# Optimization experiments

Measured on AMD Instinct MI355X. Metric: run time of the kernel, lower is better.

Reference implementation:

```python
import jax, jax.numpy as jnp
import numpy as np

N_NODES = 50000
N_FEAT = 128
N_BLOCKS = 4
N_EDGES = 800000  # ~avg degree 16 per hop
OUT_FEAT = 128


def setup_inputs() -> dict:
    key = jax.random.key(0)
    k1, k2, k3, k4, k5, k6 = jax.random.split(key, 6)
    x = jax.random.normal(k1, (N_NODES, N_FEAT), dtype=jnp.float32)
    edge_rows = jax.random.randint(k2, (N_BLOCKS, N_EDGES), 0, N_NODES, dtype=jnp.int64)
    edge_cols = jax.random.randint(k3, (N_BLOCKS, N_EDGES), 0, N_NODES, dtype=jnp.int64)
    edge_vals = jax.random.uniform(k4, (N_BLOCKS, N_EDGES), dtype=jnp.float32)
    shared_weight = jax.random.normal(k5, (N_FEAT * N_BLOCKS, OUT_FEAT), dtype=jnp.float32) * (1.0 / np.sqrt(OUT_FEAT))
    output_bias = jax.random.normal(k6, (OUT_FEAT,), dtype=jnp.float32) * (1.0 / np.sqrt(OUT_FEAT))
    return {"x": x, "edge_rows": edge_rows, "edge_cols": edge_cols,
            "edge_vals": edge_vals, "shared_weight": shared_weight,
            "output_bias": output_bias}


def reference(x, edge_rows, edge_cols, edge_vals, shared_weight, output_bias):
    # Per-hop spmm: AX_i[r] = sum_e vals[e] * x[cols[e]] scattered to rows[e]
    n = x.shape[0]

    def spmm(rows, cols, vals):
        return jax.ops.segment_sum(vals[:, None] * x[cols], rows, num_segments=n)

    hops = jax.vmap(spmm)(edge_rows, edge_cols, edge_vals)  # [B, N, F]
    # torch.cat(feature_output, 1) -> [N, B*F] with hop-major feature blocks
    cat = jnp.transpose(hops, (1, 0, 2)).reshape(n, -1)
    return cat @ shared_weight + output_bias
```

## Files before the change

### kernel.cpp

```cpp
#include <hip/hip_runtime.h>
#include <hip/hip_bf16.h>
#include <type_traits>


#define NBUK_MAX 800
#define RCAP 8192
#define NBLK 512

typedef __attribute__((ext_vector_type(8))) short short8;
typedef __attribute__((ext_vector_type(4))) float f32x4;

static __device__ __forceinline__ ushort f2bf(float f) {
  __hip_bfloat16 h = __float2bfloat16(f);
  return *(ushort*)&h;
}
static __device__ __forceinline__ float bf2f(ushort u) {
  return __uint_as_float(((unsigned)u) << 16);
}

__global__ __launch_bounds__(256) void hist2_kernel(
    const int* __restrict__ rows, int* __restrict__ cnt,
    int* __restrict__ cnt2, unsigned ntot, int nbuk, unsigned chunk)
{
  __shared__ int lcnt[NBUK_MAX];
  for (int i = threadIdx.x; i < nbuk; i += 256) lcnt[i] = 0;
  __syncthreads();
  const unsigned beg = blockIdx.x * chunk;
  const unsigned end = (beg + chunk < ntot) ? (beg + chunk) : ntot;
  if (beg < end) {
    const unsigned q0 = beg >> 2, q1 = end >> 2;
    for (unsigned i = q0 + threadIdx.x; i < q1; i += 256) {
      const int4 r4 = ((const int4*)rows)[i];
      atomicAdd(&lcnt[((unsigned)r4.x) >> 6], 1);
      atomicAdd(&lcnt[((unsigned)r4.y) >> 6], 1);
      atomicAdd(&lcnt[((unsigned)r4.z) >> 6], 1);
      atomicAdd(&lcnt[((unsigned)r4.w) >> 6], 1);
    }
  }
  __syncthreads();
  int* myrow = cnt2 + (size_t)blockIdx.x * nbuk;
  for (int i = threadIdx.x; i < nbuk; i += 256) {
    const int c = lcnt[i];
    myrow[i] = c;
    if (c) atomicAdd(&cnt[i], c);
  }
}

__global__ __launch_bounds__(1024) void scan2_kernel(
    const int* __restrict__ cnt, int* __restrict__ pstartX,
    int* __restrict__ row_start, int nbuk, int n, unsigned ntot)
{
  __shared__ int buf[1024];
  const int t = threadIdx.x;
  const int c = (t < nbuk) ? cnt[t] : 0;
  buf[t] = c;
  __syncthreads();
  for (int off = 1; off < 1024; off <<= 1) {
    const int add = (t >= off) ? buf[t - off] : 0;
    __syncthreads();
    buf[t] += add;
    __syncthreads();
  }
  if (t < nbuk) pstartX[t] = buf[t] - c;
  if (t == 0) row_start[n] = (int)ntot;
}

__global__ __launch_bounds__(256) void scanB_kernel(
    const int* __restrict__ cnt2, const int* __restrict__ pstartX,
    int* __restrict__ bstart2, int nbuk)
{
  const int bk = blockIdx.x * 4 + (threadIdx.x >> 6);
  if (bk >= nbuk) return;
  const int lane = threadIdx.x & 63;
  int v[8];
  int lanesum = 0;
#pragma unroll
  for (int i = 0; i < 8; ++i) {
    v[i] = cnt2[(size_t)(lane * 8 + i) * nbuk + bk];
    lanesum += v[i];
  }
  int incl = lanesum;
#pragma unroll
  for (int off = 1; off < 64; off <<= 1) {
    const int t = __shfl_up(incl, off);
    if (lane >= off) incl += t;
  }
  int run = pstartX[bk] + (incl - lanesum);
#pragma unroll
  for (int i = 0; i < 8; ++i) {
    bstart2[(size_t)(lane * 8 + i) * nbuk + bk] = run;
    run += v[i];
  }
}

__global__ __launch_bounds__(256) void bscatter2_kernel(
    const int* __restrict__ rows, const int* __restrict__ cols,
    const float* __restrict__ vals, const int* __restrict__ bstart2,
    uint2* __restrict__ staged, unsigned ntot, unsigned epb, int nbuk,
    unsigned chunk)
{
  __shared__ int bcnt[NBUK_MAX];
  __shared__ int lcur[NBUK_MAX];
  __shared__ uint2 bins[NBUK_MAX * 8];
  {
    const int* myrow = bstart2 + (size_t)blockIdx.x * nbuk;
    for (int i = threadIdx.x; i < nbuk; i += 256) {
      bcnt[i] = 0;
      lcur[i] = myrow[i];
    }
  }
  __syncthreads();

  const unsigned beg = blockIdx.x * chunk;
  const unsigned end = (beg + chunk < ntot) ? (beg + chunk) : ntot;

  auto push = [&](unsigned r, unsigned c, unsigned hop, float v) {
    const uint2 pay = make_uint2((r << 16) | c, (hop << 30) | __float_as_uint(v));
    const int bk = (int)(r >> 6);
    const int p = atomicAdd(&bcnt[bk], 1);
    if (p < 8) bins[bk * 8 + p] = pay;
    else {
      const int gp = atomicAdd(&lcur[bk], 1);
      staged[gp] = pay;
    }
  };

  for (unsigned base = beg; base < end; base += 2048) {
    const unsigned e0 = base + threadIdx.x * 8u;
    if (e0 + 7 < end) {
#pragma unroll
      for (int g = 0; g < 2; ++g) {
        const unsigned eg = e0 + (unsigned)g * 4u;
        const int4 r4 = *(const int4*)(rows + eg);
        const int4 c4 = *(const int4*)(cols + eg);
        const float4 v4 = *(const float4*)(vals + eg);
#pragma unroll
        for (int q = 0; q < 4; ++q) {
          const unsigned e = eg + q;
          const unsigned hop = (e >= 2u * epb) ? ((e >= 3u * epb) ? 3u : 2u)
                                               : ((e >= epb) ? 1u : 0u);
          push((unsigned)((&r4.x)[q]), (unsigned)((&c4.x)[q]), hop, (&v4.x)[q]);
        }
      }
    } else {
      for (unsigned e = e0; e < end && e < e0 + 8; ++e) {
        const unsigned hop = (e >= 2u * epb) ? ((e >= 3u * epb) ? 3u : 2u)
                                             : ((e >= epb) ? 1u : 0u);
        push((unsigned)rows[e], (unsigned)cols[e], hop, vals[e]);
      }
    }
    __syncthreads();
    for (int bk = threadIdx.x; bk < nbuk; bk += 256) {
      if (bcnt[bk] >= 8) {
        const int gp = lcur[bk];
        uint2* dst = staged + gp;
#pragma unroll
        for (int q = 0; q < 8; ++q) dst[q] = bins[bk * 8 + q];
        lcur[bk] = gp + 8;
        bcnt[bk] = 0;
      }
    }
    __syncthreads();
  }
  for (int bk = threadIdx.x; bk < nbuk; bk += 256) {
    const int c = bcnt[bk];
    if (c > 0) {
      const int gp = lcur[bk];
      for (int q = 0; q < c; ++q) staged[gp + q] = bins[bk * 8 + q];
    }
  }
}

__global__ __launch_bounds__(256) void prep_kernel(
    const float* __restrict__ X, const float* __restrict__ W,
    ushort* __restrict__ Xb, ushort* __restrict__ Wt, int nx8)
{
  const int t = blockIdx.x * 256 + threadIdx.x;
  if (t < nx8) {
    const float4 v0 = ((const float4*)X)[t * 2];
    const float4 v1 = ((const float4*)X)[t * 2 + 1];
    ushort4 o0, o1;
    o0.x = f2bf(v0.x); o0.y = f2bf(v0.y); o0.z = f2bf(v0.z); o0.w = f2bf(v0.w);
    o1.x = f2bf(v1.x); o1.y = f2bf(v1.y); o1.z = f2bf(v1.z); o1.w = f2bf(v1.w);
    ((ushort4*)Xb)[t * 2] = o0;
    ((ushort4*)Xb)[t * 2 + 1] = o1;
  } else if (t < nx8 + 8192) {
    const int u = t - nx8;
    const int gc = u >> 4;
    const int f0 = (u & 15) * 8;
    const float* src = W + (size_t)((gc >> 7) * 128) * 128 + (gc & 127);
    ushort4 o0, o1;
    o0.x = f2bf(src[(size_t)(f0 + 0) * 128]);
    o0.y = f2bf(src[(size_t)(f0 + 1) * 128]);
    o0.z = f2bf(src[(size_t)(f0 + 2) * 128]);
    o0.w = f2bf(src[(size_t)(f0 + 3) * 128]);
    o1.x = f2bf(src[(size_t)(f0 + 4) * 128]);
    o1.y = f2bf(src[(size_t)(f0 + 5) * 128]);
    o1.z = f2bf(src[(size_t)(f0 + 6) * 128]);
    o1.w = f2bf(src[(size_t)(f0 + 7) * 128]);
    ((ushort4*)(Wt + (size_t)gc * 128 + f0))[0] = o0;
    ((ushort4*)(Wt + (size_t)gc * 128 + f0))[1] = o1;
  }
}

__global__ __launch_bounds__(256) void mfma_gemm_kernel(
    const ushort* __restrict__ Xb, const ushort* __restrict__ Wt,
    ushort* __restrict__ Y, int n)
{
  const int w = threadIdx.x >> 6;
  const int l = threadIdx.x & 63;
  const int r16 = l & 15;
  const int kg = l >> 4;
  const int row0 = blockIdx.y * 64 + w * 16;
  const int c0 = blockIdx.x * 64;

  const int gra = min(row0 + r16, n - 1);
  const ushort* ap = Xb + (size_t)gra * 128 + kg * 8;
  const ushort* bp = Wt + (size_t)(c0 + r16) * 128 + kg * 8;

  f32x4 acc[4] = {};
#pragma unroll
  for (int k0 = 0; k0 < 128; k0 += 32) {
    const short8 a = *(const short8*)(ap + k0);
#pragma unroll
    for (int ct = 0; ct < 4; ++ct) {
      const short8 b = *(const short8*)(bp + (size_t)ct * 16 * 128 + k0);
      acc[ct] = __builtin_amdgcn_mfma_f32_16x16x32_bf16(a, b, acc[ct], 0, 0, 0);
    }
  }
  const int rs0 = row0 + kg * 4;
#pragma unroll
  for (int ct = 0; ct < 4; ++ct) {
    const int col = c0 + ct * 16 + r16;
#pragma unroll
    for (int r = 0; r < 4; ++r) {
      const int rs = rs0 + r;
      if (rs < n) Y[(size_t)rs * 512 + col] = f2bf(acc[ct][r]);
    }
  }
}

static __device__ __forceinline__ unsigned pack_ep(uint2 p) {
  const unsigned col = p.x & 0xFFFFu;
  const unsigned hop = p.y >> 30;
  const float v = __uint_as_float(p.y & 0x3FFFFFFFu);
  const unsigned vq = (unsigned)(v * 16383.f + 0.5f);
  return (vq << 18) | (col * 4u + hop);
}

__global__ __launch_bounds__(256) void reorder_kernel(
    const int* __restrict__ cnt, const int* __restrict__ pstartX,
    const uint2* __restrict__ staged, unsigned* __restrict__ ep,
    int* __restrict__ row_start, int n)
{
  __shared__ int lcnt[64], lstart[64], lcur[64];
  __shared__ unsigned lbuf[RCAP];
  const int bk = blockIdx.x;
  const int c = cnt[bk];
  const int sx = pstartX[bk];

  if (threadIdx.x < 64) lcnt[threadIdx.x] = 0;
  __syncthreads();
  for (int j = threadIdx.x; j < c; j += 256)
    atomicAdd(&lcnt[(staged[sx + j].x >> 16) & 63u], 1);
  __syncthreads();
  if (threadIdx.x == 0) {
    int a = 0;
    for (int i = 0; i < 64; ++i) { lstart[i] = a; lcur[i] = a; a += lcnt[i]; }
  }
  __syncthreads();
  if (threadIdx.x < 64) {
    const int gr = bk * 64 + threadIdx.x;
    if (gr < n) row_start[gr] = sx + lstart[threadIdx.x];
  }
  if (c <= RCAP) {
    for (int j = threadIdx.x; j < c; j += 256) {
      const uint2 p = staged[sx + j];
      const unsigned rl = (p.x >> 16) & 63u;
      const int pos = atomicAdd(&lcur[rl], 1);
      lbuf[pos] = pack_ep(p);
    }
    __syncthreads();
    for (int j = threadIdx.x; j < c; j += 256) ep[sx + j] = lbuf[j];
  } else {
    for (int j = threadIdx.x; j < c; j += 256) {
      const uint2 p = staged[sx + j];
      const unsigned rl = (p.x >> 16) & 63u;
      const int pos = atomicAdd(&lcur[rl], 1);
      ep[sx + pos] = pack_ep(p);
    }
  }
}

__global__ __launch_bounds__(256) void gather_kernel(
    const int* __restrict__ row_start, const unsigned* __restrict__ ep,
    const ushort* __restrict__ Y, const float* __restrict__ bias,
    float* __restrict__ out, int n)
{
  const int wid = (int)((blockIdx.x * 256u + threadIdx.x) >> 6);
  if (wid >= n) return;
  const int lane = threadIdx.x & 63;
  const int half = lane >> 5;
  const int l32 = lane & 31;
  const int js = row_start[wid];
  const int je = row_start[wid + 1];
  float a0 = 0.f, a1 = 0.f, a2 = 0.f, a3 = 0.f;

  auto acc1 = [&](unsigned p) {
    const size_t yoff = (size_t)(p & 0x3FFFFu) * 128u + l32 * 4;
    const ushort4 h = *(const ushort4*)(Y + yoff);
    const float v = (float)(p >> 18) * (1.f / 16383.f);
    a0 = fmaf(v, bf2f(h.x), a0);
    a1 = fmaf(v, bf2f(h.y), a1);
    a2 = fmaf(v, bf2f(h.z), a2);
    a3 = fmaf(v, bf2f(h.w), a3);
  };

  int j = js;
  for (; j + 7 < je; j += 8) {
    const unsigned p0 = ep[j + half];
    const unsigned p1 = ep[j + 2 + half];
    const unsigned p2 = ep[j + 4 + half];
    const unsigned p3 = ep[j + 6 + half];
    acc1(p0); acc1(p1); acc1(p2); acc1(p3);
  }
  for (; j + 1 < je; j += 2) acc1(ep[j + half]);
  if (j < je && half == 0) acc1(ep[j]);

  a0 += __shfl_xor(a0, 32);
  a1 += __shfl_xor(a1, 32);
  a2 += __shfl_xor(a2, 32);
  a3 += __shfl_xor(a3, 32);
  if (half == 0) {
    const float4 bb = ((const float4*)bias)[l32];
    *(float4*)(out + (size_t)wid * 128 + l32 * 4) =
        make_float4(a0 + bb.x, a1 + bb.y, a2 + bb.z, a3 + bb.w);
  }
}

template <typename YT>
__global__ __launch_bounds__(256, 2) void gemm_kernel(
    const float* __restrict__ X, const float* __restrict__ W,
    YT* __restrict__ Y, int n_rows, int col0, int ystride)
{
  __shared__ float Xs[64][128];
  __shared__ float Ws[128][64];
  const int tid = threadIdx.x;
  const int row0 = blockIdx.y * 64;
  {
    const int lane = tid & 31;
    const int r = tid >> 5;
#pragma unroll
    for (int i = 0; i < 8; ++i) {
      const int rr = r + i * 8;
      const int gr = row0 + rr;
      float4 v = make_float4(0.f, 0.f, 0.f, 0.f);
      if (gr < n_rows) v = ((const float4*)(X + (size_t)gr * 128))[lane];
      ((float4*)&Xs[rr][0])[lane ^ ((rr >> 2) & 7)] = v;
    }
  }
  {
    const int gc0 = col0 + blockIdx.x * 64;
    const int b = gc0 >> 7;
    const int cc0 = gc0 & 127;
    const float* Wb = W + (size_t)b * 128 * 128 + cc0;
    const int lane16 = tid & 15;
    const int f = tid >> 4;
#pragma unroll
    for (int i = 0; i < 8; ++i) {
      const int ff = f + i * 16;
      const float4 v = *(const float4*)(Wb + (size_t)ff * 128 + lane16 * 4);
      ((float4*)&Ws[ff][0])[lane16] = v;
    }
  }
  __syncthreads();
  const int tx = tid & 15;
  const int ty = tid >> 4;
  float acc[4][4] = {};
#pragma unroll 2
  for (int f0 = 0; f0 < 128; f0 += 4) {
    float4 a[4];
#pragma unroll
    for (int i = 0; i < 4; ++i) {
      const int r = ty * 4 + i;
      a[i] = ((const float4*)&Xs[r][0])[(f0 >> 2) ^ ((r >> 2) & 7)];
    }
#pragma unroll
    for (int k = 0; k < 4; ++k) {
      const float4 b = *(const float4*)&Ws[f0 + k][tx * 4];
#pragma unroll
      for (int i = 0; i < 4; ++i) {
        const float av = (&a[i].x)[k];
        acc[i][0] = fmaf(av, b.x, acc[i][0]);
        acc[i][1] = fmaf(av, b.y, acc[i][1]);
        acc[i][2] = fmaf(av, b.z, acc[i][2]);
        acc[i][3] = fmaf(av, b.w, acc[i][3]);
      }
    }
  }
  const int yc = blockIdx.x * 64 + tx * 4;
#pragma unroll
  for (int i = 0; i < 4; ++i) {
    const int gr = row0 + ty * 4 + i;
    if (gr >= n_rows) continue;
    *(float4*)(Y + (size_t)gr * ystride + yc) =
        make_float4(acc[i][0], acc[i][1], acc[i][2], acc[i][3]);
  }
}

__global__ __launch_bounds__(256) void init_out_kernel(
    float* __restrict__ out, const float* __restrict__ bias, int nquads)
{
  int i = blockIdx.x * blockDim.x + threadIdx.x;
  if (i >= nquads) return;
  const float4 b = ((const float4*)bias)[i & 31];
  ((float4*)out)[i] = b;
}

__global__ __launch_bounds__(256) void scatter_kernel(
    const int* __restrict__ rows, const int* __restrict__ cols,
    const float* __restrict__ vals, const float* __restrict__ Y,
    int ystride, int yblk, unsigned epb, unsigned ntot,
    float* __restrict__ out)
{
  const unsigned e = blockIdx.x * 8u + (threadIdx.x >> 5);
  if (e >= ntot) return;
  const int lane = threadIdx.x & 31;
  const int row = rows[e];
  const int col = cols[e];
  const float v = vals[e];
  const unsigned b = e / epb;
  const float4 y = *(const float4*)(Y + (size_t)col * ystride + (size_t)b * yblk + lane * 4);
  float* o = out + (size_t)row * 128 + lane * 4;
  atomicAdd(o + 0, v * y.x);
  atomicAdd(o + 1, v * y.y);
  atomicAdd(o + 2, v * y.z);
  atomicAdd(o + 3, v * y.w);
}

extern "C" void kernel_launch(void* const* d_in, const int* in_sizes, int n_in,
                              void* d_out, int out_size, void* d_ws, size_t ws_size,
                              hipStream_t stream) {
  const float* X    = (const float*)d_in[0];
  const int*   rows = (const int*)d_in[1];
  const int*   cols = (const int*)d_in[2];
  const float* vals = (const float*)d_in[3];
  const float* W    = (const float*)d_in[4];
  const float* bias = (const float*)d_in[5];
  float* out = (float*)d_out;

  const int n = out_size / 128;
  const unsigned ntot = (unsigned)in_sizes[1];
  const unsigned epb = ntot / 4u;
  const int nbuk = (n + 63) >> 6;

  auto align = [](size_t x) { return (x + 255) & ~(size_t)255; };
  const size_t sz_cnt    = align((size_t)nbuk * 4);
  const size_t sz_px     = align((size_t)nbuk * 4);
  const size_t sz_rstart = align((size_t)(n + 1) * 4);
  const size_t sz_cnt2   = align((size_t)NBLK * nbuk * 4);
  const size_t sz_bst2   = align((size_t)NBLK * nbuk * 4);
  const size_t sz_staged = align((size_t)ntot * 8 + 256);
  const size_t sz_ep     = align((size_t)ntot * 4);
  const size_t sz_y      = align((size_t)n * 512 * 2);
  const size_t sz_xb     = align((size_t)n * 128 * 2);
  const size_t sz_wt     = align((size_t)512 * 128 * 2);
  const size_t meta = sz_cnt + sz_px + sz_rstart + sz_cnt2 + sz_bst2 + sz_staged + sz_ep;

  char* ws = (char*)d_ws;
  int*      cnt       = (int*)(ws);
  int*      pstartX   = (int*)(ws + sz_cnt);
  int*      row_start = (int*)(ws + sz_cnt + sz_px);
  int*      cnt2      = (int*)(ws + sz_cnt + sz_px + sz_rstart);
  int*      bstart2   = (int*)(ws + sz_cnt + sz_px + sz_rstart + sz_cnt2);
  uint2*    staged    = (uint2*)(ws + sz_cnt + sz_px + sz_rstart + sz_cnt2 + sz_bst2);
  unsigned* ep        = (unsigned*)(ws + meta - sz_ep);
  ushort*   Y         = (ushort*)(ws + meta);
  ushort*   Xb        = (ushort*)(ws + meta + sz_y);
  ushort*   Wt        = (ushort*)(ws + meta + sz_y + sz_xb);

  const bool fast_ok = (n <= 65536) && (nbuk <= NBUK_MAX) && (nbuk <= 1024) &&
                       (ntot % 4u == 0u) && (in_sizes[0] == n * 128) &&
                       (in_sizes[4] == 512 * 128) &&
                       (ws_size >= meta + sz_y + sz_xb + sz_wt);

  if (fast_ok) {
    const unsigned chunk = (((ntot + NBLK - 1u) / NBLK) + 7u) & ~7u;
    hipMemsetAsync(cnt, 0, (size_t)nbuk * 4, stream);
    hist2_kernel<<<dim3(NBLK), dim3(256), 0, stream>>>(
        rows, cnt, cnt2, ntot, nbuk, chunk);
    scan2_kernel<<<dim3(1), dim3(1024), 0, stream>>>(
        cnt, pstartX, row_start, nbuk, n, ntot);
    scanB_kernel<<<dim3((nbuk + 3) / 4), dim3(256), 0, stream>>>(
        cnt2, pstartX, bstart2, nbuk);
    bscatter2_kernel<<<dim3(NBLK), dim3(256), 0, stream>>>(
        rows, cols, vals, bstart2, staged, ntot, epb, nbuk, chunk);
    reorder_kernel<<<dim3(nbuk), dim3(256), 0, stream>>>(
        cnt, pstartX, staged, ep, row_start, n);
    const int nx8 = n * 16;
    prep_kernel<<<dim3((nx8 + 8192 + 255) / 256), dim3(256), 0, stream>>>(
        X, W, Xb, Wt, nx8);
    mfma_gemm_kernel<<<dim3(8, (n + 63) / 64), dim3(256), 0, stream>>>(
        Xb, Wt, Y, n);
    const unsigned gblk = (unsigned)((n + 3) / 4);
    gather_kernel<<<dim3(gblk), dim3(256), 0, stream>>>(
        row_start, ep, Y, bias, out, n);
    return;
  }

  {
    const int nquads = n * 32;
    init_out_kernel<<<dim3((nquads + 255) / 256), dim3(256), 0, stream>>>(out, bias, nquads);
    float* Yf = (float*)d_ws;
    const size_t need_fused = (size_t)n * 512 * sizeof(float);
    if (ws_size >= need_fused) {
      dim3 g(512 / 64, (n + 63) / 64);
      gemm_kernel<float><<<g, dim3(256), 0, stream>>>(X, W, Yf, n, 0, 512);
      const unsigned nblk = (ntot + 7) / 8;
      scatter_kernel<<<dim3(nblk), dim3(256), 0, stream>>>(
          rows, cols, vals, Yf, 512, 128, epb, ntot, out);
    } else {
      for (unsigned b = 0; b < 4; ++b) {
        dim3 g(128 / 64, (n + 63) / 64);
        gemm_kernel<float><<<g, dim3(256), 0, stream>>>(X, W, Yf, n, (int)(b * 128), 128);
        const unsigned nblk = (epb + 7) / 8;
        scatter_kernel<<<dim3(nblk), dim3(256), 0, stream>>>(
            rows + (size_t)b * epb, cols + (size_t)b * epb, vals + (size_t)b * epb,
            Yf, 128, 0, epb, epb, out);
      }
    }
  }
}
```

Baseline: 249.0 us.

## Merge independent kernels into shared launches and widen gather loads to 16 bytes

The X/W bf16 conversion now runs in extra blocks of the histogram launch, and the MFMA GEMM runs in extra blocks of the reorder launch. Independent work shares a grid, which removes two launches and lets the stages overlap. The gather kernel now splits each row's edges across four 16-lane groups, each loading 8 bf16 values per edge, then reduces with two xor shuffles. The cost is more registers in the gather, and the merged blocks share one shared-memory footprint (the large reorder buffer), which may lower occupancy for the GEMM blocks.

```diff
diff --git a/kernel.cpp b/kernel.cpp
--- a/kernel.cpp
+++ b/kernel.cpp
@@ -8,6 +8,7 @@
 #define NBLK 512
 
 typedef __attribute__((ext_vector_type(8))) short short8;
+typedef __attribute__((ext_vector_type(8))) unsigned short ushort8;
 typedef __attribute__((ext_vector_type(4))) float f32x4;
 
 static __device__ __forceinline__ ushort f2bf(float f) {
@@ -18,31 +19,63 @@
   return __uint_as_float(((unsigned)u) << 16);
 }
 
-__global__ __launch_bounds__(256) void hist2_kernel(
+__global__ __launch_bounds__(256) void histprep_kernel(
     const int* __restrict__ rows, int* __restrict__ cnt,
-    int* __restrict__ cnt2, unsigned ntot, int nbuk, unsigned chunk)
+    int* __restrict__ cnt2,
+    const float* __restrict__ X, const float* __restrict__ W,
+    ushort* __restrict__ Xb, ushort* __restrict__ Wt,
+    unsigned ntot, int nbuk, unsigned chunk, int nx8)
 {
   __shared__ int lcnt[NBUK_MAX];
-  for (int i = threadIdx.x; i < nbuk; i += 256) lcnt[i] = 0;
-  __syncthreads();
-  const unsigned beg = blockIdx.x * chunk;
-  const unsigned end = (beg + chunk < ntot) ? (beg + chunk) : ntot;
-  if (beg < end) {
-    const unsigned q0 = beg >> 2, q1 = end >> 2;
-    for (unsigned i = q0 + threadIdx.x; i < q1; i += 256) {
-      const int4 r4 = ((const int4*)rows)[i];
-      atomicAdd(&lcnt[((unsigned)r4.x) >> 6], 1);
-      atomicAdd(&lcnt[((unsigned)r4.y) >> 6], 1);
-      atomicAdd(&lcnt[((unsigned)r4.z) >> 6], 1);
-      atomicAdd(&lcnt[((unsigned)r4.w) >> 6], 1);
-    }
-  }
-  __syncthreads();
-  int* myrow = cnt2 + (size_t)blockIdx.x * nbuk;
-  for (int i = threadIdx.x; i < nbuk; i += 256) {
-    const int c = lcnt[i];
-    myrow[i] = c;
-    if (c) atomicAdd(&cnt[i], c);
+  if (blockIdx.x < NBLK) {
+    for (int i = threadIdx.x; i < nbuk; i += 256) lcnt[i] = 0;
+    __syncthreads();
+    const unsigned beg = blockIdx.x * chunk;
+    const unsigned end = (beg + chunk < ntot) ? (beg + chunk) : ntot;
+    if (beg < end) {
+      const unsigned q0 = beg >> 2, q1 = end >> 2;
+      for (unsigned i = q0 + threadIdx.x; i < q1; i += 256) {
+        const int4 r4 = ((const int4*)rows)[i];
+        atomicAdd(&lcnt[((unsigned)r4.x) >> 6], 1);
+        atomicAdd(&lcnt[((unsigned)r4.y) >> 6], 1);
+        atomicAdd(&lcnt[((unsigned)r4.z) >> 6], 1);
+        atomicAdd(&lcnt[((unsigned)r4.w) >> 6], 1);
+      }
+    }
+    __syncthreads();
+    int* myrow = cnt2 + (size_t)blockIdx.x * nbuk;
+    for (int i = threadIdx.x; i < nbuk; i += 256) {
+      const int c = lcnt[i];
+      myrow[i] = c;
+      if (c) atomicAdd(&cnt[i], c);
+    }
+  } else {
+    const int t = (blockIdx.x - NBLK) * 256 + threadIdx.x;
+    if (t < nx8) {
+      const float4 v0 = ((const float4*)X)[t * 2];
+      const float4 v1 = ((const float4*)X)[t * 2 + 1];
+      ushort4 o0, o1;
+      o0.x = f2bf(v0.x); o0.y = f2bf(v0.y); o0.z = f2bf(v0.z); o0.w = f2bf(v0.w);
+      o1.x = f2bf(v1.x); o1.y = f2bf(v1.y); o1.z = f2bf(v1.z); o1.w = f2bf(v1.w);
+      ((ushort4*)Xb)[t * 2] = o0;
+      ((ushort4*)Xb)[t * 2 + 1] = o1;
+    } else if (t < nx8 + 8192) {
+      const int u = t - nx8;
+      const int gc = u >> 4;
+      const int f0 = (u & 15) * 8;
+      const float* src = W + (size_t)((gc >> 7) * 128) * 128 + (gc & 127);
+      ushort4 o0, o1;
+      o0.x = f2bf(src[(size_t)(f0 + 0) * 128]);
+      o0.y = f2bf(src[(size_t)(f0 + 1) * 128]);
+      o0.z = f2bf(src[(size_t)(f0 + 2) * 128]);
+      o0.w = f2bf(src[(size_t)(f0 + 3) * 128]);
+      o1.x = f2bf(src[(size_t)(f0 + 4) * 128]);
+      o1.y = f2bf(src[(size_t)(f0 + 5) * 128]);
+      o1.z = f2bf(src[(size_t)(f0 + 6) * 128]);
+      o1.w = f2bf(src[(size_t)(f0 + 7) * 128]);
+      ((ushort4*)(Wt + (size_t)gc * 128 + f0))[0] = o0;
+      ((ushort4*)(Wt + (size_t)gc * 128 + f0))[1] = o1;
+    }
   }
 }
 
@@ -171,75 +204,6 @@
   }
 }
 
-__global__ __launch_bounds__(256) void prep_kernel(
-    const float* __restrict__ X, const float* __restrict__ W,
-    ushort* __restrict__ Xb, ushort* __restrict__ Wt, int nx8)
-{
-  const int t = blockIdx.x * 256 + threadIdx.x;
-  if (t < nx8) {
-    const float4 v0 = ((const float4*)X)[t * 2];
-    const float4 v1 = ((const float4*)X)[t * 2 + 1];
-    ushort4 o0, o1;
-    o0.x = f2bf(v0.x); o0.y = f2bf(v0.y); o0.z = f2bf(v0.z); o0.w = f2bf(v0.w);
-    o1.x = f2bf(v1.x); o1.y = f2bf(v1.y); o1.z = f2bf(v1.z); o1.w = f2bf(v1.w);
-    ((ushort4*)Xb)[t * 2] = o0;
-    ((ushort4*)Xb)[t * 2 + 1] = o1;
-  } else if (t < nx8 + 8192) {
-    const int u = t - nx8;
-    const int gc = u >> 4;
-    const int f0 = (u & 15) * 8;
-    const float* src = W + (size_t)((gc >> 7) * 128) * 128 + (gc & 127);
-    ushort4 o0, o1;
-    o0.x = f2bf(src[(size_t)(f0 + 0) * 128]);
-    o0.y = f2bf(src[(size_t)(f0 + 1) * 128]);
-    o0.z = f2bf(src[(size_t)(f0 + 2) * 128]);
-    o0.w = f2bf(src[(size_t)(f0 + 3) * 128]);
-    o1.x = f2bf(src[(size_t)(f0 + 4) * 128]);
-    o1.y = f2bf(src[(size_t)(f0 + 5) * 128]);
-    o1.z = f2bf(src[(size_t)(f0 + 6) * 128]);
-    o1.w = f2bf(src[(size_t)(f0 + 7) * 128]);
-    ((ushort4*)(Wt + (size_t)gc * 128 + f0))[0] = o0;
-    ((ushort4*)(Wt + (size_t)gc * 128 + f0))[1] = o1;
-  }
-}
-
-__global__ __launch_bounds__(256) void mfma_gemm_kernel(
-    const ushort* __restrict__ Xb, const ushort* __restrict__ Wt,
-    ushort* __restrict__ Y, int n)
-{
-  const int w = threadIdx.x >> 6;
-  const int l = threadIdx.x & 63;
-  const int r16 = l & 15;
-  const int kg = l >> 4;
-  const int row0 = blockIdx.y * 64 + w * 16;
-  const int c0 = blockIdx.x * 64;
-
-  const int gra = min(row0 + r16, n - 1);
-  const ushort* ap = Xb + (size_t)gra * 128 + kg * 8;
-  const ushort* bp = Wt + (size_t)(c0 + r16) * 128 + kg * 8;
-
-  f32x4 acc[4] = {};
-#pragma unroll
-  for (int k0 = 0; k0 < 128; k0 += 32) {
-    const short8 a = *(const short8*)(ap + k0);
-#pragma unroll
-    for (int ct = 0; ct < 4; ++ct) {
-      const short8 b = *(const short8*)(bp + (size_t)ct * 16 * 128 + k0);
-      acc[ct] = __builtin_amdgcn_mfma_f32_16x16x32_bf16(a, b, acc[ct], 0, 0, 0);
-    }
-  }
-  const int rs0 = row0 + kg * 4;
-#pragma unroll
-  for (int ct = 0; ct < 4; ++ct) {
-    const int col = c0 + ct * 16 + r16;
-#pragma unroll
-    for (int r = 0; r < 4; ++r) {
-      const int rs = rs0 + r;
-      if (rs < n) Y[(size_t)rs * 512 + col] = f2bf(acc[ct][r]);
-    }
-  }
-}
-
 static __device__ __forceinline__ unsigned pack_ep(uint2 p) {
   const unsigned col = p.x & 0xFFFFu;
   const unsigned hop = p.y >> 30;
@@ -248,46 +212,86 @@
   return (vq << 18) | (col * 4u + hop);
 }
 
-__global__ __launch_bounds__(256) void reorder_kernel(
+__global__ __launch_bounds__(256) void reordmm_kernel(
     const int* __restrict__ cnt, const int* __restrict__ pstartX,
     const uint2* __restrict__ staged, unsigned* __restrict__ ep,
-    int* __restrict__ row_start, int n)
+    int* __restrict__ row_start,
+    const ushort* __restrict__ Xb, const ushort* __restrict__ Wt,
+    ushort* __restrict__ Y, int n, int nbuk)
 {
   __shared__ int lcnt[64], lstart[64], lcur[64];
   __shared__ unsigned lbuf[RCAP];
-  const int bk = blockIdx.x;
-  const int c = cnt[bk];
-  const int sx = pstartX[bk];
-
-  if (threadIdx.x < 64) lcnt[threadIdx.x] = 0;
-  __syncthreads();
-  for (int j = threadIdx.x; j < c; j += 256)
-    atomicAdd(&lcnt[(staged[sx + j].x >> 16) & 63u], 1);
-  __syncthreads();
-  if (threadIdx.x == 0) {
-    int a = 0;
-    for (int i = 0; i < 64; ++i) { lstart[i] = a; lcur[i] = a; a += lcnt[i]; }
-  }
-  __syncthreads();
-  if (threadIdx.x < 64) {
-    const int gr = bk * 64 + threadIdx.x;
-    if (gr < n) row_start[gr] = sx + lstart[threadIdx.x];
-  }
-  if (c <= RCAP) {
-    for (int j = threadIdx.x; j < c; j += 256) {
-      const uint2 p = staged[sx + j];
-      const unsigned rl = (p.x >> 16) & 63u;
-      const int pos = atomicAdd(&lcur[rl], 1);
-      lbuf[pos] = pack_ep(p);
-    }
-    __syncthreads();
-    for (int j = threadIdx.x; j < c; j += 256) ep[sx + j] = lbuf[j];
+
+  if (blockIdx.x < (unsigned)nbuk) {
+    const int bk = blockIdx.x;
+    const int c = cnt[bk];
+    const int sx = pstartX[bk];
+
+    if (threadIdx.x < 64) lcnt[threadIdx.x] = 0;
+    __syncthreads();
+    for (int j = threadIdx.x; j < c; j += 256)
+      atomicAdd(&lcnt[(staged[sx + j].x >> 16) & 63u], 1);
+    __syncthreads();
+    if (threadIdx.x == 0) {
+      int a = 0;
+      for (int i = 0; i < 64; ++i) { lstart[i] = a; lcur[i] = a; a += lcnt[i]; }
+    }
+    __syncthreads();
+    if (threadIdx.x < 64) {
+      const int gr = bk * 64 + threadIdx.x;
+      if (gr < n) row_start[gr] = sx + lstart[threadIdx.x];
+    }
+    if (c <= RCAP) {
+      for (int j = threadIdx.x; j < c; j += 256) {
+        const uint2 p = staged[sx + j];
+        const unsigned rl = (p.x >> 16) & 63u;
+        const int pos = atomicAdd(&lcur[rl], 1);
+        lbuf[pos] = pack_ep(p);
+      }
+      __syncthreads();
+      for (int j = threadIdx.x; j < c; j += 256) ep[sx + j] = lbuf[j];
+    } else {
+      for (int j = threadIdx.x; j < c; j += 256) {
+        const uint2 p = staged[sx + j];
+        const unsigned rl = (p.x >> 16) & 63u;
+        const int pos = atomicAdd(&lcur[rl], 1);
+        ep[sx + pos] = pack_ep(p);
+      }
+    }
   } else {
-    for (int j = threadIdx.x; j < c; j += 256) {
-      const uint2 p = staged[sx + j];
-      const unsigned rl = (p.x >> 16) & 63u;
-      const int pos = atomicAdd(&lcur[rl], 1);
-      ep[sx + pos] = pack_ep(p);
+    const int u = (int)blockIdx.x - nbuk;
+    const int bx = u & 7;
+    const int by = u >> 3;
+    const int w = threadIdx.x >> 6;
+    const int l = threadIdx.x & 63;
+    const int r16 = l & 15;
+    const int kg = l >> 4;
+    const int row0 = by * 64 + w * 16;
+    const int c0 = bx * 64;
+
+    const int gra = min(row0 + r16, n - 1);
+    const ushort* ap = Xb + (size_t)gra * 128 + kg * 8;
+    const ushort* bp = Wt + (size_t)(c0 + r16) * 128 + kg * 8;
+
+    f32x4 acc[4] = {};
+#pragma unroll
+    for (int k0 = 0; k0 < 128; k0 += 32) {
+      const short8 a = *(const short8*)(ap + k0);
+#pragma unroll
+      for (int ct = 0; ct < 4; ++ct) {
+        const short8 b = *(const short8*)(bp + (size_t)ct * 16 * 128 + k0);
+        acc[ct] = __builtin_amdgcn_mfma_f32_16x16x32_bf16(a, b, acc[ct], 0, 0, 0);
+      }
+    }
+    const int rs0 = row0 + kg * 4;
+#pragma unroll
+    for (int ct = 0; ct < 4; ++ct) {
+      const int col = c0 + ct * 16 + r16;
+#pragma unroll
+      for (int r = 0; r < 4; ++r) {
+        const int rs = rs0 + r;
+        if (rs < n) Y[(size_t)rs * 512 + col] = f2bf(acc[ct][r]);
+      }
     }
   }
 }
@@ -300,41 +304,44 @@
   const int wid = (int)((blockIdx.x * 256u + threadIdx.x) >> 6);
   if (wid >= n) return;
   const int lane = threadIdx.x & 63;
-  const int half = lane >> 5;
-  const int l32 = lane & 31;
+  const int qw = lane >> 4;
+  const int l16 = lane & 15;
   const int js = row_start[wid];
   const int je = row_start[wid + 1];
-  float a0 = 0.f, a1 = 0.f, a2 = 0.f, a3 = 0.f;
+  float a[8];
+#pragma unroll
+  for (int k = 0; k < 8; ++k) a[k] = 0.f;
 
   auto acc1 = [&](unsigned p) {
-    const size_t yoff = (size_t)(p & 0x3FFFFu) * 128u + l32 * 4;
-    const ushort4 h = *(const ushort4*)(Y + yoff);
+    const ushort8 h = *(const ushort8*)(Y + (size_t)(p & 0x3FFFFu) * 128u + l16 * 8);
     const float v = (float)(p >> 18) * (1.f / 16383.f);
-    a0 = fmaf(v, bf2f(h.x), a0);
-    a1 = fmaf(v, bf2f(h.y), a1);
-    a2 = fmaf(v, bf2f(h.z), a2);
-    a3 = fmaf(v, bf2f(h.w), a3);
+#pragma unroll
+    for (int k = 0; k < 8; ++k) a[k] = fmaf(v, bf2f(h[k]), a[k]);
   };
 
   int j = js;
-  for (; j + 7 < je; j += 8) {
-    const unsigned p0 = ep[j + half];
-    const unsigned p1 = ep[j + 2 + half];
-    const unsigned p2 = ep[j + 4 + half];
-    const unsigned p3 = ep[j + 6 + half];
+  for (; j + 15 < je; j += 16) {
+    const unsigned p0 = ep[j + qw];
+    const unsigned p1 = ep[j + 4 + qw];
+    const unsigned p2 = ep[j + 8 + qw];
+    const unsigned p3 = ep[j + 12 + qw];
     acc1(p0); acc1(p1); acc1(p2); acc1(p3);
   }
-  for (; j + 1 < je; j += 2) acc1(ep[j + half]);
-  if (j < je && half == 0) acc1(ep[j]);
-
-  a0 += __shfl_xor(a0, 32);
-  a1 += __shfl_xor(a1, 32);
-  a2 += __shfl_xor(a2, 32);
-  a3 += __shfl_xor(a3, 32);
-  if (half == 0) {
-    const float4 bb = ((const float4*)bias)[l32];
-    *(float4*)(out + (size_t)wid * 128 + l32 * 4) =
-        make_float4(a0 + bb.x, a1 + bb.y, a2 + bb.z, a3 + bb.w);
+  for (; j + 3 < je; j += 4) acc1(ep[j + qw]);
+  const int rem = je - j;
+  if (qw < rem) acc1(ep[j + qw]);
+
+#pragma unroll
+  for (int k = 0; k < 8; ++k) {
+    a[k] += __shfl_xor(a[k], 16);
+    a[k] += __shfl_xor(a[k], 32);
+  }
+  if (qw == 0) {
+    const float4 b0 = ((const float4*)bias)[l16 * 2];
+    const float4 b1 = ((const float4*)bias)[l16 * 2 + 1];
+    float* o = out + (size_t)wid * 128 + l16 * 8;
+    *(float4*)(o)     = make_float4(a[0] + b0.x, a[1] + b0.y, a[2] + b0.z, a[3] + b0.w);
+    *(float4*)(o + 4) = make_float4(a[4] + b1.x, a[5] + b1.y, a[6] + b1.z, a[7] + b1.w);
   }
 }
 
@@ -486,22 +493,20 @@
 
   if (fast_ok) {
     const unsigned chunk = (((ntot + NBLK - 1u) / NBLK) + 7u) & ~7u;
+    const int nx8 = n * 16;
+    const int nprep = (nx8 + 8192 + 255) / 256;
     hipMemsetAsync(cnt, 0, (size_t)nbuk * 4, stream);
-    hist2_kernel<<<dim3(NBLK), dim3(256), 0, stream>>>(
-        rows, cnt, cnt2, ntot, nbuk, chunk);
+    histprep_kernel<<<dim3(NBLK + nprep), dim3(256), 0, stream>>>(
+        rows, cnt, cnt2, X, W, Xb, Wt, ntot, nbuk, chunk, nx8);
     scan2_kernel<<<dim3(1), dim3(1024), 0, stream>>>(
         cnt, pstartX, row_start, nbuk, n, ntot);
     scanB_kernel<<<dim3((nbuk + 3) / 4), dim3(256), 0, stream>>>(
         cnt2, pstartX, bstart2, nbuk);
     bscatter2_kernel<<<dim3(NBLK), dim3(256), 0, stream>>>(
         rows, cols, vals, bstart2, staged, ntot, epb, nbuk, chunk);
-    reorder_kernel<<<dim3(nbuk), dim3(256), 0, stream>>>(
-        cnt, pstartX, staged, ep, row_start, n);
-    const int nx8 = n * 16;
-    prep_kernel<<<dim3((nx8 + 8192 + 255) / 256), dim3(256), 0, stream>>>(
-        X, W, Xb, Wt, nx8);
-    mfma_gemm_kernel<<<dim3(8, (n + 63) / 64), dim3(256), 0, stream>>>(
-        Xb, Wt, Y, n);
+    const int nby = (n + 63) / 64;
+    reordmm_kernel<<<dim3(nbuk + 8 * nby), dim3(256), 0, stream>>>(
+        cnt, pstartX, staged, ep, row_start, Xb, Wt, Y, n, nbuk);
     const unsigned gblk = (unsigned)((n + 3) / 4);
     gather_kernel<<<dim3(gblk), dim3(256), 0, stream>>>(
         row_start, ep, Y, bias, out, n);
```

Result: faster. 238.1 us (-4.4%).
